# Performance work log

Measured on AMD Instinct MI355X. Metric: run time of the kernel, lower is better.

Reference implementation:

```python
import jax, jax.numpy as jnp
import numpy as np

N = 50000      # nodes
E = 600000     # edges (avg degree 12)
D = 128        # in_dim == hidden_dim
C = 47         # n_classes
L = 3          # n_layers


def setup_inputs() -> dict:
    key = jax.random.key(0)
    ks = jax.random.split(key, 8)
    s = 1.0 / np.sqrt(D)
    return {
        "features": jax.random.normal(ks[0], (N, D), jnp.float32),
        "src": jax.random.randint(ks[1], (E,), 0, N, jnp.int32),
        "dst": jax.random.randint(ks[2], (E,), 0, N, jnp.int32),
        "w_self": jax.random.normal(ks[3], (L, D, D), jnp.float32) * s,
        "w_neigh": jax.random.normal(ks[4], (L, D, D), jnp.float32) * s,
        "b": jax.random.normal(ks[5], (L, D), jnp.float32) * s,
        "wc": jax.random.normal(ks[6], (D, C), jnp.float32) * s,
        "bc": jax.random.normal(ks[7], (C,), jnp.float32) * s,
    }


def reference(features, src, dst, w_self, w_neigh, b, wc, bc):
    # in-degree for mean aggregation (clamped to avoid div-by-zero)
    deg = jax.ops.segment_sum(jnp.ones((E,), features.dtype), dst, num_segments=N)
    inv_deg = 1.0 / jnp.maximum(deg, 1.0)  # [N]
    h = features
    for l in range(L):
        # SAGEConv (mean aggregator): gather src feats, mean-reduce onto dst
        msgs = jnp.take(h, src, axis=0)                       # [E, D]
        h_neigh = jax.ops.segment_sum(msgs, dst, num_segments=N) * inv_deg[:, None]  # [N, D]
        h = jax.nn.relu(h @ w_self[l] + h_neigh @ w_neigh[l] + b[l])
    logits = h @ wc + bc                                      # [N, C]
    return jax.nn.softmax(logits, axis=-1)
```

## Files before the change

kernel.cpp:

```cpp
#include <hip/hip_runtime.h>
#include <hip/hip_bf16.h>
#include <float.h>

#define DIM  128
#define NCLS 47
#define MAXD 64

typedef __attribute__((ext_vector_type(8))) short bf16x8;
typedef __attribute__((ext_vector_type(4))) float f32x4;
typedef unsigned short u16;

__device__ inline unsigned short bf16_rne(float v) {
  unsigned u = __float_as_uint(v);
  return (unsigned short)((u + 0x7FFFu + ((u >> 16) & 1u)) >> 16);
}

__device__ inline void split_bf16(float v, unsigned short& hi, unsigned short& lo) {
  unsigned int u = __float_as_uint(v);
  unsigned int r = (u + 0x7FFFu + ((u >> 16) & 1u)) >> 16;
  hi = (unsigned short)r;
  float hf = __uint_as_float(r << 16);
  float l = v - hf;
  unsigned int ul = __float_as_uint(l);
  unsigned int rl = (ul + 0x7FFFu + ((ul >> 16) & 1u)) >> 16;
  lo = (unsigned short)rl;
}

__device__ inline uint4 pack8(const unsigned short* h) {
  uint4 u;
  u.x = (unsigned)h[0] | ((unsigned)h[1] << 16);
  u.y = (unsigned)h[2] | ((unsigned)h[3] << 16);
  u.z = (unsigned)h[4] | ((unsigned)h[5] << 16);
  u.w = (unsigned)h[6] | ((unsigned)h[7] << 16);
  return u;
}

__global__ __launch_bounds__(256) void k_init(u16* __restrict__ eidx,
                                              int* __restrict__ cnt,
                                              u16* __restrict__ P0,
                                              u16* __restrict__ P1,
                                              u16* __restrict__ P2,
                                              int n, long t8) {
  long i = (long)blockIdx.x * 256 + threadIdx.x;
  if (i < t8) {
    unsigned s2 = (unsigned)n | ((unsigned)n << 16);
    uint4 v = {s2, s2, s2, s2};
    ((uint4*)eidx)[i] = v;
  }
  if (i < n) cnt[i] = 0;
  if (i < 16) {
    uint4 z = {0u, 0u, 0u, 0u};
    ((uint4*)(P0 + (size_t)n * DIM))[i] = z;
    ((uint4*)(P1 + (size_t)n * DIM))[i] = z;
    ((uint4*)(P2 + (size_t)n * DIM))[i] = z;
  }
}

__global__ __launch_bounds__(256) void k_prep(const float* __restrict__ w_self,
                                              const float* __restrict__ w_neigh,
                                              const float* __restrict__ wc,
                                              const float* __restrict__ feat,
                                              const int* __restrict__ src,
                                              const int* __restrict__ dst,
                                              uint4* __restrict__ Bhi,
                                              uint4* __restrict__ Blo,
                                              uint4* __restrict__ Chi,
                                              uint4* __restrict__ Clo,
                                              unsigned short* __restrict__ P0,
                                              int* __restrict__ cnt,
                                              u16* __restrict__ eidx,
                                              int n, long total8, int E, int nS) {
  int bid = blockIdx.x, tid = threadIdx.x;
  if (bid < nS) {
    int t = bid * 256 + tid;
    int e0 = t * 4;
    if (e0 + 3 < E) {
      int4 d4 = *(const int4*)(dst + e0);
      int4 s4 = *(const int4*)(src + e0);
      int p0 = atomicAdd(&cnt[d4.x], 1);
      int p1 = atomicAdd(&cnt[d4.y], 1);
      int p2 = atomicAdd(&cnt[d4.z], 1);
      int p3 = atomicAdd(&cnt[d4.w], 1);
      if (p0 < MAXD) eidx[(size_t)d4.x * MAXD + p0] = (u16)s4.x;
      if (p1 < MAXD) eidx[(size_t)d4.y * MAXD + p1] = (u16)s4.y;
      if (p2 < MAXD) eidx[(size_t)d4.z * MAXD + p2] = (u16)s4.z;
      if (p3 < MAXD) eidx[(size_t)d4.w * MAXD + p3] = (u16)s4.w;
    } else {
      for (int e = e0; e < E; ++e) {
        int d = dst[e];
        int pos = atomicAdd(&cnt[d], 1);
        if (pos < MAXD) eidx[(size_t)d * MAXD + pos] = (u16)src[e];
      }
    }
    return;
  }
  bid -= nS;
  if (bid < 48) {
    int unit = bid * 4 + (tid >> 6);
    int lane = tid & 63;
    int lt = unit >> 6, rem = unit & 63, kt = rem >> 3, ct = rem & 7;
    int col = ct * 16 + (lane & 15);
    unsigned short h[8], lw[8];
#pragma unroll
    for (int j = 0; j < 8; ++j) {
      int kg = kt * 32 + (lane >> 4) * 8 + j;
      float v = (kg < 128) ? w_self[(size_t)lt * DIM * DIM + (size_t)kg * DIM + col]
                           : w_neigh[(size_t)lt * DIM * DIM + (size_t)(kg - 128) * DIM + col];
      split_bf16(v, h[j], lw[j]);
    }
    size_t idx = (((size_t)lt * 64 + kt * 8 + ct) * 64 + lane);
    Bhi[idx] = pack8(h);
    Blo[idx] = pack8(lw);
  } else if (bid < 51) {
    int unit = (bid - 48) * 4 + (tid >> 6);
    if (unit < 12) {
      int lane = tid & 63;
      int kt = unit / 3, ct = unit % 3;
      int col = ct * 16 + (lane & 15);
      unsigned short h[8], lw[8];
#pragma unroll
      for (int j = 0; j < 8; ++j) {
        int k = kt * 32 + (lane >> 4) * 8 + j;
        float v = (col < NCLS) ? wc[(size_t)k * NCLS + col] : 0.f;
        split_bf16(v, h[j], lw[j]);
      }
      size_t idx = (size_t)(kt * 3 + ct) * 64 + lane;
      Chi[idx] = pack8(h);
      Clo[idx] = pack8(lw);
    }
  } else {
    long i = (long)(bid - 51) * 256 + tid;
    if (i < total8) {
      const float* s = feat + i * 8;
      unsigned short h[8];
#pragma unroll
      for (int j = 0; j < 8; ++j) h[j] = bf16_rne(s[j]);
      *(uint4*)&P0[i * 8] = pack8(h);
    }
  }
}

__global__ __launch_bounds__(256) void k_agg9(const unsigned short* __restrict__ plane,
                                              unsigned short* __restrict__ hn,
                                              const int* __restrict__ cnt,
                                              const u16* __restrict__ eidx, int n) {
  int node = blockIdx.x * 4 + (threadIdx.x >> 6);
  if (node >= n) return;
  int lane = threadIdx.x & 63;
  int g = lane >> 4, li = lane & 15;
  int d = cnt[node];
  int dcl = d < MAXD ? d : MAXD;
  int s = node * MAXD;
  int nch = (dcl + 15) >> 4;
  float acc[8];
#pragma unroll
  for (int k = 0; k < 8; ++k) acc[k] = 0.f;

  for (int c = 0; c < nch; ++c) {
    int base = s + c * 16 + g;
    int u0 = eidx[base];
    int u1 = eidx[base + 4];
    int u2 = eidx[base + 8];
    int u3 = eidx[base + 12];
    uint4 v0 = *(const uint4*)(plane + (size_t)u0 * DIM + li * 8);
    uint4 v1 = *(const uint4*)(plane + (size_t)u1 * DIM + li * 8);
    uint4 v2 = *(const uint4*)(plane + (size_t)u2 * DIM + li * 8);
    uint4 v3 = *(const uint4*)(plane + (size_t)u3 * DIM + li * 8);
    acc[0] += __uint_as_float(v0.x << 16); acc[1] += __uint_as_float(v0.x & 0xffff0000u);
    acc[2] += __uint_as_float(v0.y << 16); acc[3] += __uint_as_float(v0.y & 0xffff0000u);
    acc[4] += __uint_as_float(v0.z << 16); acc[5] += __uint_as_float(v0.z & 0xffff0000u);
    acc[6] += __uint_as_float(v0.w << 16); acc[7] += __uint_as_float(v0.w & 0xffff0000u);
    acc[0] += __uint_as_float(v1.x << 16); acc[1] += __uint_as_float(v1.x & 0xffff0000u);
    acc[2] += __uint_as_float(v1.y << 16); acc[3] += __uint_as_float(v1.y & 0xffff0000u);
    acc[4] += __uint_as_float(v1.z << 16); acc[5] += __uint_as_float(v1.z & 0xffff0000u);
    acc[6] += __uint_as_float(v1.w << 16); acc[7] += __uint_as_float(v1.w & 0xffff0000u);
    acc[0] += __uint_as_float(v2.x << 16); acc[1] += __uint_as_float(v2.x & 0xffff0000u);
    acc[2] += __uint_as_float(v2.y << 16); acc[3] += __uint_as_float(v2.y & 0xffff0000u);
    acc[4] += __uint_as_float(v2.z << 16); acc[5] += __uint_as_float(v2.z & 0xffff0000u);
    acc[6] += __uint_as_float(v2.w << 16); acc[7] += __uint_as_float(v2.w & 0xffff0000u);
    acc[0] += __uint_as_float(v3.x << 16); acc[1] += __uint_as_float(v3.x & 0xffff0000u);
    acc[2] += __uint_as_float(v3.y << 16); acc[3] += __uint_as_float(v3.y & 0xffff0000u);
    acc[4] += __uint_as_float(v3.z << 16); acc[5] += __uint_as_float(v3.z & 0xffff0000u);
    acc[6] += __uint_as_float(v3.w << 16); acc[7] += __uint_as_float(v3.w & 0xffff0000u);
  }
#pragma unroll
  for (int k = 0; k < 8; ++k) {
    acc[k] += __shfl_xor(acc[k], 16);
    acc[k] += __shfl_xor(acc[k], 32);
  }
  if (g == 0) {
    float idg = 1.0f / (float)(d > 1 ? d : 1);
    unsigned short hb[8];
#pragma unroll
    for (int k = 0; k < 8; ++k) hb[k] = bf16_rne(acc[k] * idg);
    *(uint4*)(hn + (size_t)node * DIM + li * 8) = pack8(hb);
  }
}

template <int LAST>
__global__ __launch_bounds__(256) void k_mm2(const unsigned short* __restrict__ plane,
                                             const unsigned short* __restrict__ hn,
                                             const uint4* __restrict__ Bhi,
                                             const uint4* __restrict__ Blo,
                                             const float* __restrict__ bias,
                                             unsigned short* __restrict__ oplane,
                                             const uint4* __restrict__ Chi,
                                             const uint4* __restrict__ Clo,
                                             const float* __restrict__ bc,
                                             float* __restrict__ out,
                                             int n) {
  __shared__ char U[34816];
  uint4* Bs = (uint4*)U;
  int tid = threadIdx.x, lane = tid & 63, w = tid >> 6;
  int rb = blockIdx.x * 128 + w * 32;

  f32x4 acc[2][8];
#pragma unroll
  for (int rf = 0; rf < 2; ++rf)
#pragma unroll
    for (int ct = 0; ct < 8; ++ct) acc[rf][ct] = (f32x4){0.f, 0.f, 0.f, 0.f};

  int r0 = rb + (lane & 15);      if (r0 > n - 1) r0 = n - 1;
  int r1 = rb + 16 + (lane & 15); if (r1 > n - 1) r1 = n - 1;
  int koff = (lane >> 4) * 8;
  const unsigned short* a0s = plane + (size_t)r0 * DIM + koff;
  const unsigned short* a1s = plane + (size_t)r1 * DIM + koff;
  const unsigned short* a0n = hn + (size_t)r0 * DIM + koff;
  const unsigned short* a1n = hn + (size_t)r1 * DIM + koff;

#define STAGE_B(kt_, buf_)                                                    \
  {                                                                           \
    const uint4* hsrc = Bhi + (size_t)(kt_) * 512;                            \
    const uint4* lsrc = Blo + (size_t)(kt_) * 512;                            \
    uint4* dstb = Bs + (size_t)(buf_) * 1024;                                 \
    dstb[tid]        = hsrc[tid];                                             \
    dstb[tid + 256]  = hsrc[tid + 256];                                       \
    dstb[tid + 512]  = lsrc[tid];                                             \
    dstb[tid + 768]  = lsrc[tid + 256];                                       \
  }

  STAGE_B(0, 0);
  __syncthreads();

#pragma unroll
  for (int kt = 0; kt < 8; ++kt) {
    if (kt < 7) STAGE_B(kt + 1, (kt + 1) & 1);
    int buf = kt & 1;
    bf16x8 a0 = (kt < 4) ? *(const bf16x8*)(a0s + kt * 32)
                         : *(const bf16x8*)(a0n + (kt - 4) * 32);
    bf16x8 a1 = (kt < 4) ? *(const bf16x8*)(a1s + kt * 32)
                         : *(const bf16x8*)(a1n + (kt - 4) * 32);
    const uint4* bb = Bs + (size_t)buf * 1024;
#pragma unroll
    for (int ct = 0; ct < 8; ++ct) {
      bf16x8 bh = *(const bf16x8*)&bb[ct * 64 + lane];
      bf16x8 bl = *(const bf16x8*)&bb[512 + ct * 64 + lane];
      acc[0][ct] = __builtin_amdgcn_mfma_f32_16x16x32_bf16(a0, bh, acc[0][ct], 0, 0, 0);
      acc[0][ct] = __builtin_amdgcn_mfma_f32_16x16x32_bf16(a0, bl, acc[0][ct], 0, 0, 0);
      acc[1][ct] = __builtin_amdgcn_mfma_f32_16x16x32_bf16(a1, bh, acc[1][ct], 0, 0, 0);
      acc[1][ct] = __builtin_amdgcn_mfma_f32_16x16x32_bf16(a1, bl, acc[1][ct], 0, 0, 0);
    }
    __syncthreads();
  }
#undef STAGE_B

  char* tw = U + (size_t)w * 32 * 272;
#pragma unroll
  for (int rf = 0; rf < 2; ++rf)
#pragma unroll
    for (int ct = 0; ct < 8; ++ct) {
      float bv = bias[ct * 16 + (lane & 15)];
#pragma unroll
      for (int q = 0; q < 4; ++q) {
        float val = fmaxf(acc[rf][ct][q] + bv, 0.f);
        int row = rf * 16 + (lane >> 4) * 4 + q;
        int key = ((row >> 2) & 3) << 5;
        int cb = (ct * 32 + (lane & 15) * 2) ^ key;
        *(unsigned short*)(tw + row * 272 + cb) = bf16_rne(val);
      }
    }

  if (!LAST) {
#pragma unroll
    for (int rr = 0; rr < 2; ++rr) {
      int r = rr * 16 + (lane >> 2);
      int grow = rb + r;
      if (grow < n) {
        int key = ((r >> 2) & 3) << 5;
        int cb0 = (lane & 3) * 64;
#pragma unroll
        for (int j = 0; j < 4; ++j) {
          uint4 v = *(const uint4*)(tw + r * 272 + ((cb0 + j * 16) ^ key));
          *(uint4*)(oplane + (size_t)grow * DIM + (cb0 + j * 16) / 2) = v;
        }
      }
    }
  } else {
#pragma unroll
    for (int rf = 0; rf < 2; ++rf) {
      f32x4 cacc[3];
#pragma unroll
      for (int ct = 0; ct < 3; ++ct) cacc[ct] = (f32x4){0.f, 0.f, 0.f, 0.f};
      int row = rf * 16 + (lane & 15);
      int key = ((row >> 2) & 3) << 5;
#pragma unroll
      for (int kt = 0; kt < 4; ++kt) {
        int bo = (kt * 64 + (lane >> 4) * 16) ^ key;
        bf16x8 a = *(const bf16x8*)(tw + row * 272 + bo);
#pragma unroll
        for (int ct = 0; ct < 3; ++ct) {
          bf16x8 bh = *(const bf16x8*)&Chi[(size_t)(kt * 3 + ct) * 64 + lane];
          bf16x8 bl = *(const bf16x8*)&Clo[(size_t)(kt * 3 + ct) * 64 + lane];
          cacc[ct] = __builtin_amdgcn_mfma_f32_16x16x32_bf16(a, bh, cacc[ct], 0, 0, 0);
          cacc[ct] = __builtin_amdgcn_mfma_f32_16x16x32_bf16(a, bl, cacc[ct], 0, 0, 0);
        }
      }
      int c0 = (lane & 15);
      int c1 = 16 + (lane & 15);
      int c2 = 32 + (lane & 15);
      bool v2 = c2 < NCLS;
      float b0 = bc[c0], b1 = bc[c1], b2 = v2 ? bc[c2] : 0.f;
#pragma unroll
      for (int q = 0; q < 4; ++q) {
        int grow = rb + rf * 16 + (lane >> 4) * 4 + q;
        float l0 = cacc[0][q] + b0;
        float l1 = cacc[1][q] + b1;
        float l2 = v2 ? cacc[2][q] + b2 : -FLT_MAX;
        float m = fmaxf(l0, fmaxf(l1, l2));
#pragma unroll
        for (int off = 8; off >= 1; off >>= 1) m = fmaxf(m, __shfl_xor(m, off));
        float e0 = __expf(l0 - m);
        float e1 = __expf(l1 - m);
        float e2 = v2 ? __expf(l2 - m) : 0.f;
        float sden = e0 + e1 + e2;
#pragma unroll
        for (int off = 8; off >= 1; off >>= 1) sden += __shfl_xor(sden, off);
        float inv = 1.0f / sden;
        if (grow < n) {
          out[(size_t)grow * NCLS + c0] = e0 * inv;
          out[(size_t)grow * NCLS + c1] = e1 * inv;
          if (v2) out[(size_t)grow * NCLS + c2] = e2 * inv;
        }
      }
    }
  }
}

extern "C" void kernel_launch(void* const* d_in, const int* in_sizes, int n_in,
                              void* d_out, int out_size, void* d_ws, size_t ws_size,
                              hipStream_t stream) {
  const float* feat   = (const float*)d_in[0];
  const int*   src    = (const int*)d_in[1];
  const int*   dst    = (const int*)d_in[2];
  const float* w_self = (const float*)d_in[3];
  const float* w_neigh= (const float*)d_in[4];
  const float* b      = (const float*)d_in[5];
  const float* wc     = (const float*)d_in[6];
  const float* bc     = (const float*)d_in[7];
  float* out = (float*)d_out;

  const int N = in_sizes[0] / DIM;
  const int E = in_sizes[1];
  const size_t PS  = (size_t)N * DIM;
  const size_t PSP = (size_t)(N + 1) * DIM;

  unsigned short* P0 = (unsigned short*)d_ws;
  unsigned short* P1 = P0 + PSP;
  unsigned short* P2 = P1 + PSP;
  unsigned short* HN = P2 + PSP;
  int*   cnt  = (int*)(HN + PS);
  u16*   eidx = (u16*)(cnt + N);
  uintptr_t aln = ((uintptr_t)(eidx + (size_t)N * MAXD) + 255) & ~(uintptr_t)255;
  uint4* Bhi = (uint4*)aln;
  uint4* Blo = Bhi + 3 * 4096;
  uint4* Chi = Blo + 3 * 4096;
  uint4* Clo = Chi + 12 * 64;

  long t8 = (long)N * MAXD / 8;
  int nInit = (int)((t8 + 255) / 256);
  k_init<<<nInit, 256, 0, stream>>>(eidx, cnt, P0, P1, P2, N, t8);

  long total8 = (long)(PS / 8);
  int nCvt = (int)((total8 + 255) / 256);
  int nE4 = (E + 3) / 4;
  int nS = (nE4 + 255) / 256;
  k_prep<<<nS + 51 + nCvt, 256, 0, stream>>>(w_self, w_neigh, wc, feat, src, dst,
                                             Bhi, Blo, Chi, Clo, P0,
                                             cnt, eidx, N, total8, E, nS);

  const unsigned short* hin = P0;
  unsigned short* houts[2] = {P1, P2};
  for (int l = 0; l < 3; ++l) {
    k_agg9<<<(N + 3) / 4, 256, 0, stream>>>(hin, HN, cnt, eidx, N);
    if (l < 2) {
      k_mm2<0><<<(N + 127) / 128, 256, 0, stream>>>(hin, HN,
          Bhi + (size_t)l * 4096, Blo + (size_t)l * 4096,
          b + (size_t)l * DIM, houts[l], Chi, Clo, bc, out, N);
      hin = houts[l];
    } else {
      k_mm2<1><<<(N + 127) / 128, 256, 0, stream>>>(hin, HN,
          Bhi + (size_t)l * 4096, Blo + (size_t)l * 4096,
          b + (size_t)l * DIM, (unsigned short*)nullptr, Chi, Clo, bc, out, N);
    }
  }
}
```

Before: 177.2 us.

## Bucket neighbor lists by source-id range to improve gather locality

Each destination's neighbor list is now split into 8 buckets keyed on the high bits of the source id (16 slots each), with per-bucket atomic counters replacing the single counter. The aggregation kernel walks the buckets in order, so concurrently running wavefronts tend to gather from similar source-id ranges, which should improve L2 locality of feature reads. In exchange the index array and counters get larger, the per-node init work grows, and the inner gather loop loses its 4-way unrolled independent loads. Edges overflowing a 16-slot bucket are dropped, and nodes with more than 8 buckets' worth of ids (N beyond 65536) would overflow the layout.

```diff
diff --git a/kernel.cpp b/kernel.cpp
--- a/kernel.cpp
+++ b/kernel.cpp
@@ -2,9 +2,11 @@
 #include <hip/hip_bf16.h>
 #include <float.h>
 
-#define DIM  128
-#define NCLS 47
-#define MAXD 64
+#define DIM   128
+#define NCLS  47
+#define NBKT  8
+#define BSLOT 16
+#define SLOTS 128
 
 typedef __attribute__((ext_vector_type(8))) short bf16x8;
 typedef __attribute__((ext_vector_type(4))) float f32x4;
@@ -36,7 +38,7 @@
 }
 
 __global__ __launch_bounds__(256) void k_init(u16* __restrict__ eidx,
-                                              int* __restrict__ cnt,
+                                              int* __restrict__ cnt8,
                                               u16* __restrict__ P0,
                                               u16* __restrict__ P1,
                                               u16* __restrict__ P2,
@@ -47,7 +49,7 @@
     uint4 v = {s2, s2, s2, s2};
     ((uint4*)eidx)[i] = v;
   }
-  if (i < n) cnt[i] = 0;
+  if (i < (long)n * NBKT) cnt8[i] = 0;
   if (i < 16) {
     uint4 z = {0u, 0u, 0u, 0u};
     ((uint4*)(P0 + (size_t)n * DIM))[i] = z;
@@ -67,7 +69,7 @@
                                               uint4* __restrict__ Chi,
                                               uint4* __restrict__ Clo,
                                               unsigned short* __restrict__ P0,
-                                              int* __restrict__ cnt,
+                                              int* __restrict__ cnt8,
                                               u16* __restrict__ eidx,
                                               int n, long total8, int E, int nS) {
   int bid = blockIdx.x, tid = threadIdx.x;
@@ -77,19 +79,21 @@
     if (e0 + 3 < E) {
       int4 d4 = *(const int4*)(dst + e0);
       int4 s4 = *(const int4*)(src + e0);
-      int p0 = atomicAdd(&cnt[d4.x], 1);
-      int p1 = atomicAdd(&cnt[d4.y], 1);
-      int p2 = atomicAdd(&cnt[d4.z], 1);
-      int p3 = atomicAdd(&cnt[d4.w], 1);
-      if (p0 < MAXD) eidx[(size_t)d4.x * MAXD + p0] = (u16)s4.x;
-      if (p1 < MAXD) eidx[(size_t)d4.y * MAXD + p1] = (u16)s4.y;
-      if (p2 < MAXD) eidx[(size_t)d4.z * MAXD + p2] = (u16)s4.z;
-      if (p3 < MAXD) eidx[(size_t)d4.w * MAXD + p3] = (u16)s4.w;
+      int b0 = s4.x >> 13, b1 = s4.y >> 13, b2 = s4.z >> 13, b3 = s4.w >> 13;
+      int p0 = atomicAdd(&cnt8[(size_t)d4.x * NBKT + b0], 1);
+      int p1 = atomicAdd(&cnt8[(size_t)d4.y * NBKT + b1], 1);
+      int p2 = atomicAdd(&cnt8[(size_t)d4.z * NBKT + b2], 1);
+      int p3 = atomicAdd(&cnt8[(size_t)d4.w * NBKT + b3], 1);
+      if (p0 < BSLOT) eidx[(size_t)d4.x * SLOTS + b0 * BSLOT + p0] = (u16)s4.x;
+      if (p1 < BSLOT) eidx[(size_t)d4.y * SLOTS + b1 * BSLOT + p1] = (u16)s4.y;
+      if (p2 < BSLOT) eidx[(size_t)d4.z * SLOTS + b2 * BSLOT + p2] = (u16)s4.z;
+      if (p3 < BSLOT) eidx[(size_t)d4.w * SLOTS + b3 * BSLOT + p3] = (u16)s4.w;
     } else {
       for (int e = e0; e < E; ++e) {
-        int d = dst[e];
-        int pos = atomicAdd(&cnt[d], 1);
-        if (pos < MAXD) eidx[(size_t)d * MAXD + pos] = (u16)src[e];
+        int d = dst[e], s = src[e];
+        int b = s >> 13;
+        int pos = atomicAdd(&cnt8[(size_t)d * NBKT + b], 1);
+        if (pos < BSLOT) eidx[(size_t)d * SLOTS + b * BSLOT + pos] = (u16)s;
       }
     }
     return;
@@ -140,48 +144,39 @@
   }
 }
 
-__global__ __launch_bounds__(256) void k_agg9(const unsigned short* __restrict__ plane,
+__global__ __launch_bounds__(256) void k_aggB(const unsigned short* __restrict__ plane,
                                               unsigned short* __restrict__ hn,
-                                              const int* __restrict__ cnt,
-                                              const u16* __restrict__ eidx, int n) {
+                                              const int* __restrict__ cnt8,
+                                              const u16* __restrict__ eidx,
+                                              int n, int nb) {
   int node = blockIdx.x * 4 + (threadIdx.x >> 6);
   if (node >= n) return;
   int lane = threadIdx.x & 63;
   int g = lane >> 4, li = lane & 15;
-  int d = cnt[node];
-  int dcl = d < MAXD ? d : MAXD;
-  int s = node * MAXD;
-  int nch = (dcl + 15) >> 4;
+  const int* cb = cnt8 + (size_t)node * NBKT;
+  int c[NBKT];
+  int d = 0;
+#pragma unroll
+  for (int b = 0; b < NBKT; ++b) { c[b] = cb[b]; d += c[b]; }
+
   float acc[8];
 #pragma unroll
   for (int k = 0; k < 8; ++k) acc[k] = 0.f;
 
-  for (int c = 0; c < nch; ++c) {
-    int base = s + c * 16 + g;
-    int u0 = eidx[base];
-    int u1 = eidx[base + 4];
-    int u2 = eidx[base + 8];
-    int u3 = eidx[base + 12];
-    uint4 v0 = *(const uint4*)(plane + (size_t)u0 * DIM + li * 8);
-    uint4 v1 = *(const uint4*)(plane + (size_t)u1 * DIM + li * 8);
-    uint4 v2 = *(const uint4*)(plane + (size_t)u2 * DIM + li * 8);
-    uint4 v3 = *(const uint4*)(plane + (size_t)u3 * DIM + li * 8);
-    acc[0] += __uint_as_float(v0.x << 16); acc[1] += __uint_as_float(v0.x & 0xffff0000u);
-    acc[2] += __uint_as_float(v0.y << 16); acc[3] += __uint_as_float(v0.y & 0xffff0000u);
-    acc[4] += __uint_as_float(v0.z << 16); acc[5] += __uint_as_float(v0.z & 0xffff0000u);
-    acc[6] += __uint_as_float(v0.w << 16); acc[7] += __uint_as_float(v0.w & 0xffff0000u);
-    acc[0] += __uint_as_float(v1.x << 16); acc[1] += __uint_as_float(v1.x & 0xffff0000u);
-    acc[2] += __uint_as_float(v1.y << 16); acc[3] += __uint_as_float(v1.y & 0xffff0000u);
-    acc[4] += __uint_as_float(v1.z << 16); acc[5] += __uint_as_float(v1.z & 0xffff0000u);
-    acc[6] += __uint_as_float(v1.w << 16); acc[7] += __uint_as_float(v1.w & 0xffff0000u);
-    acc[0] += __uint_as_float(v2.x << 16); acc[1] += __uint_as_float(v2.x & 0xffff0000u);
-    acc[2] += __uint_as_float(v2.y << 16); acc[3] += __uint_as_float(v2.y & 0xffff0000u);
-    acc[4] += __uint_as_float(v2.z << 16); acc[5] += __uint_as_float(v2.z & 0xffff0000u);
-    acc[6] += __uint_as_float(v2.w << 16); acc[7] += __uint_as_float(v2.w & 0xffff0000u);
-    acc[0] += __uint_as_float(v3.x << 16); acc[1] += __uint_as_float(v3.x & 0xffff0000u);
-    acc[2] += __uint_as_float(v3.y << 16); acc[3] += __uint_as_float(v3.y & 0xffff0000u);
-    acc[4] += __uint_as_float(v3.z << 16); acc[5] += __uint_as_float(v3.z & 0xffff0000u);
-    acc[6] += __uint_as_float(v3.w << 16); acc[7] += __uint_as_float(v3.w & 0xffff0000u);
+  int base = node * SLOTS;
+  for (int b = 0; b < nb; ++b) {
+    int cbk = c[b];
+    if (cbk == 0) continue;
+    int cc = cbk < BSLOT ? cbk : BSLOT;
+    int sb = base + b * BSLOT + g;
+    for (int c0 = 0; c0 < cc; c0 += 4) {
+      int u = eidx[sb + c0];
+      uint4 v = *(const uint4*)(plane + (size_t)u * DIM + li * 8);
+      acc[0] += __uint_as_float(v.x << 16); acc[1] += __uint_as_float(v.x & 0xffff0000u);
+      acc[2] += __uint_as_float(v.y << 16); acc[3] += __uint_as_float(v.y & 0xffff0000u);
+      acc[4] += __uint_as_float(v.z << 16); acc[5] += __uint_as_float(v.z & 0xffff0000u);
+      acc[6] += __uint_as_float(v.w << 16); acc[7] += __uint_as_float(v.w & 0xffff0000u);
+    }
   }
 #pragma unroll
   for (int k = 0; k < 8; ++k) {
@@ -368,17 +363,17 @@
   unsigned short* P1 = P0 + PSP;
   unsigned short* P2 = P1 + PSP;
   unsigned short* HN = P2 + PSP;
-  int*   cnt  = (int*)(HN + PS);
-  u16*   eidx = (u16*)(cnt + N);
-  uintptr_t aln = ((uintptr_t)(eidx + (size_t)N * MAXD) + 255) & ~(uintptr_t)255;
+  int*   cnt8 = (int*)(HN + PS);
+  u16*   eidx = (u16*)(cnt8 + (size_t)N * NBKT);
+  uintptr_t aln = ((uintptr_t)(eidx + (size_t)N * SLOTS) + 255) & ~(uintptr_t)255;
   uint4* Bhi = (uint4*)aln;
   uint4* Blo = Bhi + 3 * 4096;
   uint4* Chi = Blo + 3 * 4096;
   uint4* Clo = Chi + 12 * 64;
 
-  long t8 = (long)N * MAXD / 8;
+  long t8 = (long)N * SLOTS / 8;
   int nInit = (int)((t8 + 255) / 256);
-  k_init<<<nInit, 256, 0, stream>>>(eidx, cnt, P0, P1, P2, N, t8);
+  k_init<<<nInit, 256, 0, stream>>>(eidx, cnt8, P0, P1, P2, N, t8);
 
   long total8 = (long)(PS / 8);
   int nCvt = (int)((total8 + 255) / 256);
@@ -386,12 +381,13 @@
   int nS = (nE4 + 255) / 256;
   k_prep<<<nS + 51 + nCvt, 256, 0, stream>>>(w_self, w_neigh, wc, feat, src, dst,
                                              Bhi, Blo, Chi, Clo, P0,
-                                             cnt, eidx, N, total8, E, nS);
-
+                                             cnt8, eidx, N, total8, E, nS);
+
+  int nb = (N + 8191) >> 13;
   const unsigned short* hin = P0;
   unsigned short* houts[2] = {P1, P2};
   for (int l = 0; l < 3; ++l) {
-    k_agg9<<<(N + 3) / 4, 256, 0, stream>>>(hin, HN, cnt, eidx, N);
+    k_aggB<<<(N + 3) / 4, 256, 0, stream>>>(hin, HN, cnt8, eidx, N, nb);
     if (l < 2) {
       k_mm2<0><<<(N + 127) / 128, 256, 0, stream>>>(hin, HN,
           Bhi + (size_t)l * 4096, Blo + (size_t)l * 4096,
```

Result: slower. 236.6 us (+33.6%).

## Fuse neighbor mean aggregation into the MFMA layer kernel via LDS

Applied to the files above, without the earlier changes.

Removes the separate aggregation kernel. Each 128-row matmul block now gathers and mean-reduces its own nodes' neighbor features and writes the result into a swizzled LDS tile, which then feeds the second half of the K loop. This drops the global write and read of the aggregated buffer and three kernel launches. In exchange, LDS per block grows to 64KB and the gather runs on only a few hundred blocks, with each wave handling two nodes at a time. That cuts occupancy and the parallelism available to hide gather latency.

```diff
diff --git a/kernel.cpp b/kernel.cpp
--- a/kernel.cpp
+++ b/kernel.cpp
@@ -140,93 +140,31 @@
   }
 }
 
-__global__ __launch_bounds__(256) void k_agg9(const unsigned short* __restrict__ plane,
-                                              unsigned short* __restrict__ hn,
-                                              const int* __restrict__ cnt,
-                                              const u16* __restrict__ eidx, int n) {
-  int node = blockIdx.x * 4 + (threadIdx.x >> 6);
-  if (node >= n) return;
-  int lane = threadIdx.x & 63;
-  int g = lane >> 4, li = lane & 15;
-  int d = cnt[node];
-  int dcl = d < MAXD ? d : MAXD;
-  int s = node * MAXD;
-  int nch = (dcl + 15) >> 4;
-  float acc[8];
-#pragma unroll
-  for (int k = 0; k < 8; ++k) acc[k] = 0.f;
-
-  for (int c = 0; c < nch; ++c) {
-    int base = s + c * 16 + g;
-    int u0 = eidx[base];
-    int u1 = eidx[base + 4];
-    int u2 = eidx[base + 8];
-    int u3 = eidx[base + 12];
-    uint4 v0 = *(const uint4*)(plane + (size_t)u0 * DIM + li * 8);
-    uint4 v1 = *(const uint4*)(plane + (size_t)u1 * DIM + li * 8);
-    uint4 v2 = *(const uint4*)(plane + (size_t)u2 * DIM + li * 8);
-    uint4 v3 = *(const uint4*)(plane + (size_t)u3 * DIM + li * 8);
-    acc[0] += __uint_as_float(v0.x << 16); acc[1] += __uint_as_float(v0.x & 0xffff0000u);
-    acc[2] += __uint_as_float(v0.y << 16); acc[3] += __uint_as_float(v0.y & 0xffff0000u);
-    acc[4] += __uint_as_float(v0.z << 16); acc[5] += __uint_as_float(v0.z & 0xffff0000u);
-    acc[6] += __uint_as_float(v0.w << 16); acc[7] += __uint_as_float(v0.w & 0xffff0000u);
-    acc[0] += __uint_as_float(v1.x << 16); acc[1] += __uint_as_float(v1.x & 0xffff0000u);
-    acc[2] += __uint_as_float(v1.y << 16); acc[3] += __uint_as_float(v1.y & 0xffff0000u);
-    acc[4] += __uint_as_float(v1.z << 16); acc[5] += __uint_as_float(v1.z & 0xffff0000u);
-    acc[6] += __uint_as_float(v1.w << 16); acc[7] += __uint_as_float(v1.w & 0xffff0000u);
-    acc[0] += __uint_as_float(v2.x << 16); acc[1] += __uint_as_float(v2.x & 0xffff0000u);
-    acc[2] += __uint_as_float(v2.y << 16); acc[3] += __uint_as_float(v2.y & 0xffff0000u);
-    acc[4] += __uint_as_float(v2.z << 16); acc[5] += __uint_as_float(v2.z & 0xffff0000u);
-    acc[6] += __uint_as_float(v2.w << 16); acc[7] += __uint_as_float(v2.w & 0xffff0000u);
-    acc[0] += __uint_as_float(v3.x << 16); acc[1] += __uint_as_float(v3.x & 0xffff0000u);
-    acc[2] += __uint_as_float(v3.y << 16); acc[3] += __uint_as_float(v3.y & 0xffff0000u);
-    acc[4] += __uint_as_float(v3.z << 16); acc[5] += __uint_as_float(v3.z & 0xffff0000u);
-    acc[6] += __uint_as_float(v3.w << 16); acc[7] += __uint_as_float(v3.w & 0xffff0000u);
-  }
-#pragma unroll
-  for (int k = 0; k < 8; ++k) {
-    acc[k] += __shfl_xor(acc[k], 16);
-    acc[k] += __shfl_xor(acc[k], 32);
-  }
-  if (g == 0) {
-    float idg = 1.0f / (float)(d > 1 ? d : 1);
-    unsigned short hb[8];
-#pragma unroll
-    for (int k = 0; k < 8; ++k) hb[k] = bf16_rne(acc[k] * idg);
-    *(uint4*)(hn + (size_t)node * DIM + li * 8) = pack8(hb);
-  }
-}
+#define ACC8(A, V)                                                             \
+  A[0] += __uint_as_float((V).x << 16); A[1] += __uint_as_float((V).x & 0xffff0000u); \
+  A[2] += __uint_as_float((V).y << 16); A[3] += __uint_as_float((V).y & 0xffff0000u); \
+  A[4] += __uint_as_float((V).z << 16); A[5] += __uint_as_float((V).z & 0xffff0000u); \
+  A[6] += __uint_as_float((V).w << 16); A[7] += __uint_as_float((V).w & 0xffff0000u);
 
 template <int LAST>
-__global__ __launch_bounds__(256) void k_mm2(const unsigned short* __restrict__ plane,
-                                             const unsigned short* __restrict__ hn,
-                                             const uint4* __restrict__ Bhi,
-                                             const uint4* __restrict__ Blo,
-                                             const float* __restrict__ bias,
-                                             unsigned short* __restrict__ oplane,
-                                             const uint4* __restrict__ Chi,
-                                             const uint4* __restrict__ Clo,
-                                             const float* __restrict__ bc,
-                                             float* __restrict__ out,
-                                             int n) {
-  __shared__ char U[34816];
+__global__ __launch_bounds__(256) void k_fused(const unsigned short* __restrict__ plane,
+                                               const int* __restrict__ cnt,
+                                               const u16* __restrict__ eidx,
+                                               const uint4* __restrict__ Bhi,
+                                               const uint4* __restrict__ Blo,
+                                               const float* __restrict__ bias,
+                                               unsigned short* __restrict__ oplane,
+                                               const uint4* __restrict__ Chi,
+                                               const uint4* __restrict__ Clo,
+                                               const float* __restrict__ bc,
+                                               float* __restrict__ out,
+                                               int n) {
+  __shared__ char U[65536];
   uint4* Bs = (uint4*)U;
+  char* HNl = U + 32768;
   int tid = threadIdx.x, lane = tid & 63, w = tid >> 6;
-  int rb = blockIdx.x * 128 + w * 32;
-
-  f32x4 acc[2][8];
-#pragma unroll
-  for (int rf = 0; rf < 2; ++rf)
-#pragma unroll
-    for (int ct = 0; ct < 8; ++ct) acc[rf][ct] = (f32x4){0.f, 0.f, 0.f, 0.f};
-
-  int r0 = rb + (lane & 15);      if (r0 > n - 1) r0 = n - 1;
-  int r1 = rb + 16 + (lane & 15); if (r1 > n - 1) r1 = n - 1;
-  int koff = (lane >> 4) * 8;
-  const unsigned short* a0s = plane + (size_t)r0 * DIM + koff;
-  const unsigned short* a1s = plane + (size_t)r1 * DIM + koff;
-  const unsigned short* a0n = hn + (size_t)r0 * DIM + koff;
-  const unsigned short* a1n = hn + (size_t)r1 * DIM + koff;
+  int rb = blockIdx.x * 128;
+  int wrb = rb + w * 32;
 
 #define STAGE_B(kt_, buf_)                                                    \
   {                                                                           \
@@ -240,16 +178,121 @@
   }
 
   STAGE_B(0, 0);
+
+  {
+    int g = lane >> 4, li = lane & 15;
+    for (int ii = 0; ii < 16; ++ii) {
+      int la = w * 32 + ii, lb = la + 16;
+      int na = rb + la, nb = rb + lb;
+      bool va = na < n, vb = nb < n;
+      int da = 0, db = 0;
+      uint4 av0, av1, av2, av3, bv0, bv1, bv2, bv3;
+      if (va) {
+        da = cnt[na];
+        int sa = na * MAXD + g;
+        int u0 = eidx[sa], u1 = eidx[sa + 4], u2 = eidx[sa + 8], u3 = eidx[sa + 12];
+        av0 = *(const uint4*)(plane + (size_t)u0 * DIM + li * 8);
+        av1 = *(const uint4*)(plane + (size_t)u1 * DIM + li * 8);
+        av2 = *(const uint4*)(plane + (size_t)u2 * DIM + li * 8);
+        av3 = *(const uint4*)(plane + (size_t)u3 * DIM + li * 8);
+      }
+      if (vb) {
+        db = cnt[nb];
+        int sb = nb * MAXD + g;
+        int u0 = eidx[sb], u1 = eidx[sb + 4], u2 = eidx[sb + 8], u3 = eidx[sb + 12];
+        bv0 = *(const uint4*)(plane + (size_t)u0 * DIM + li * 8);
+        bv1 = *(const uint4*)(plane + (size_t)u1 * DIM + li * 8);
+        bv2 = *(const uint4*)(plane + (size_t)u2 * DIM + li * 8);
+        bv3 = *(const uint4*)(plane + (size_t)u3 * DIM + li * 8);
+      }
+      if (va) {
+        float aa[8];
+#pragma unroll
+        for (int k = 0; k < 8; ++k) aa[k] = 0.f;
+        ACC8(aa, av0) ACC8(aa, av1) ACC8(aa, av2) ACC8(aa, av3)
+        int dcl = da < MAXD ? da : MAXD;
+        int nch = (dcl + 15) >> 4;
+        for (int c = 1; c < nch; ++c) {
+          int base = na * MAXD + c * 16 + g;
+          int u0 = eidx[base], u1 = eidx[base + 4], u2 = eidx[base + 8], u3 = eidx[base + 12];
+          uint4 v0 = *(const uint4*)(plane + (size_t)u0 * DIM + li * 8);
+          uint4 v1 = *(const uint4*)(plane + (size_t)u1 * DIM + li * 8);
+          uint4 v2 = *(const uint4*)(plane + (size_t)u2 * DIM + li * 8);
+          uint4 v3 = *(const uint4*)(plane + (size_t)u3 * DIM + li * 8);
+          ACC8(aa, v0) ACC8(aa, v1) ACC8(aa, v2) ACC8(aa, v3)
+        }
+#pragma unroll
+        for (int k = 0; k < 8; ++k) {
+          aa[k] += __shfl_xor(aa[k], 16);
+          aa[k] += __shfl_xor(aa[k], 32);
+        }
+        if (g == 0) {
+          float idg = 1.0f / (float)(da > 1 ? da : 1);
+          unsigned short hb[8];
+#pragma unroll
+          for (int k = 0; k < 8; ++k) hb[k] = bf16_rne(aa[k] * idg);
+          *(uint4*)(HNl + la * 256 + ((li * 16) ^ ((la & 7) << 4))) = pack8(hb);
+        }
+      }
+      if (vb) {
+        float ab[8];
+#pragma unroll
+        for (int k = 0; k < 8; ++k) ab[k] = 0.f;
+        ACC8(ab, bv0) ACC8(ab, bv1) ACC8(ab, bv2) ACC8(ab, bv3)
+        int dcl = db < MAXD ? db : MAXD;
+        int nch = (dcl + 15) >> 4;
+        for (int c = 1; c < nch; ++c) {
+          int base = nb * MAXD + c * 16 + g;
+          int u0 = eidx[base], u1 = eidx[base + 4], u2 = eidx[base + 8], u3 = eidx[base + 12];
+          uint4 v0 = *(const uint4*)(plane + (size_t)u0 * DIM + li * 8);
+          uint4 v1 = *(const uint4*)(plane + (size_t)u1 * DIM + li * 8);
+          uint4 v2 = *(const uint4*)(plane + (size_t)u2 * DIM + li * 8);
+          uint4 v3 = *(const uint4*)(plane + (size_t)u3 * DIM + li * 8);
+          ACC8(ab, v0) ACC8(ab, v1) ACC8(ab, v2) ACC8(ab, v3)
+        }
+#pragma unroll
+        for (int k = 0; k < 8; ++k) {
+          ab[k] += __shfl_xor(ab[k], 16);
+          ab[k] += __shfl_xor(ab[k], 32);
+        }
+        if (g == 0) {
+          float idg = 1.0f / (float)(db > 1 ? db : 1);
+          unsigned short hb[8];
+#pragma unroll
+          for (int k = 0; k < 8; ++k) hb[k] = bf16_rne(ab[k] * idg);
+          *(uint4*)(HNl + lb * 256 + ((li * 16) ^ ((lb & 7) << 4))) = pack8(hb);
+        }
+      }
+    }
+  }
   __syncthreads();
+
+  f32x4 acc[2][8];
+#pragma unroll
+  for (int rf = 0; rf < 2; ++rf)
+#pragma unroll
+    for (int ct = 0; ct < 8; ++ct) acc[rf][ct] = (f32x4){0.f, 0.f, 0.f, 0.f};
+
+  int r0 = wrb + (lane & 15);      if (r0 > n - 1) r0 = n - 1;
+  int r1 = wrb + 16 + (lane & 15); if (r1 > n - 1) r1 = n - 1;
+  int lr0 = r0 - rb, lr1 = r1 - rb;
+  int koff = (lane >> 4) * 8;
+  const unsigned short* a0s = plane + (size_t)r0 * DIM + koff;
+  const unsigned short* a1s = plane + (size_t)r1 * DIM + koff;
 
 #pragma unroll
   for (int kt = 0; kt < 8; ++kt) {
     if (kt < 7) STAGE_B(kt + 1, (kt + 1) & 1);
     int buf = kt & 1;
-    bf16x8 a0 = (kt < 4) ? *(const bf16x8*)(a0s + kt * 32)
-                         : *(const bf16x8*)(a0n + (kt - 4) * 32);
-    bf16x8 a1 = (kt < 4) ? *(const bf16x8*)(a1s + kt * 32)
-                         : *(const bf16x8*)(a1n + (kt - 4) * 32);
+    bf16x8 a0, a1;
+    if (kt < 4) {
+      a0 = *(const bf16x8*)(a0s + kt * 32);
+      a1 = *(const bf16x8*)(a1s + kt * 32);
+    } else {
+      int cb2 = koff * 2 + (kt - 4) * 64;
+      a0 = *(const bf16x8*)(HNl + lr0 * 256 + (cb2 ^ ((lr0 & 7) << 4)));
+      a1 = *(const bf16x8*)(HNl + lr1 * 256 + (cb2 ^ ((lr1 & 7) << 4)));
+    }
     const uint4* bb = Bs + (size_t)buf * 1024;
 #pragma unroll
     for (int ct = 0; ct < 8; ++ct) {
@@ -284,7 +327,7 @@
 #pragma unroll
     for (int rr = 0; rr < 2; ++rr) {
       int r = rr * 16 + (lane >> 2);
-      int grow = rb + r;
+      int grow = wrb + r;
       if (grow < n) {
         int key = ((r >> 2) & 3) << 5;
         int cb0 = (lane & 3) * 64;
@@ -322,7 +365,7 @@
       float b0 = bc[c0], b1 = bc[c1], b2 = v2 ? bc[c2] : 0.f;
 #pragma unroll
       for (int q = 0; q < 4; ++q) {
-        int grow = rb + rf * 16 + (lane >> 4) * 4 + q;
+        int grow = wrb + rf * 16 + (lane >> 4) * 4 + q;
         float l0 = cacc[0][q] + b0;
         float l1 = cacc[1][q] + b1;
         float l2 = v2 ? cacc[2][q] + b2 : -FLT_MAX;
@@ -367,8 +410,7 @@
   unsigned short* P0 = (unsigned short*)d_ws;
   unsigned short* P1 = P0 + PSP;
   unsigned short* P2 = P1 + PSP;
-  unsigned short* HN = P2 + PSP;
-  int*   cnt  = (int*)(HN + PS);
+  int*   cnt  = (int*)(P2 + PSP);
   u16*   eidx = (u16*)(cnt + N);
   uintptr_t aln = ((uintptr_t)(eidx + (size_t)N * MAXD) + 255) & ~(uintptr_t)255;
   uint4* Bhi = (uint4*)aln;
@@ -388,17 +430,17 @@
                                              Bhi, Blo, Chi, Clo, P0,
                                              cnt, eidx, N, total8, E, nS);
 
+  int nBlk = (N + 127) / 128;
   const unsigned short* hin = P0;
   unsigned short* houts[2] = {P1, P2};
   for (int l = 0; l < 3; ++l) {
-    k_agg9<<<(N + 3) / 4, 256, 0, stream>>>(hin, HN, cnt, eidx, N);
     if (l < 2) {
-      k_mm2<0><<<(N + 127) / 128, 256, 0, stream>>>(hin, HN,
+      k_fused<0><<<nBlk, 256, 0, stream>>>(hin, cnt, eidx,
           Bhi + (size_t)l * 4096, Blo + (size_t)l * 4096,
           b + (size_t)l * DIM, houts[l], Chi, Clo, bc, out, N);
       hin = houts[l];
     } else {
-      k_mm2<1><<<(N + 127) / 128, 256, 0, stream>>>(hin, HN,
+      k_fused<1><<<nBlk, 256, 0, stream>>>(hin, cnt, eidx,
           Bhi + (size_t)l * 4096, Blo + (size_t)l * 4096,
           b + (size_t)l * DIM, (unsigned short*)nullptr, Chi, Clo, bc, out, N);
     }
```

Result: slower. 220.6 us (+24.5%).

## Build neighbor lists via two-pass binned scatter with shared-memory atomics

Applied to the files above, without the earlier changes.

Replaces the direct global atomic per-edge insertion into the padded neighbor table with a two-stage binning: edges are first bucketed by dst>>8 into per-bin buffers using shared-memory histograms and one global atomic per bin per block, then a per-bin kernel assigns slots with shared atomics and writes eidx and degree counts. This aims to cut contended global atomics and scattered writes during graph preprocessing. It adds an extra kernel launch and a staging buffer with a fixed per-bin capacity that could drop edges if a bin overflows.

```diff
diff --git a/kernel.cpp b/kernel.cpp
--- a/kernel.cpp
+++ b/kernel.cpp
@@ -2,9 +2,10 @@
 #include <hip/hip_bf16.h>
 #include <float.h>
 
-#define DIM  128
-#define NCLS 47
-#define MAXD 64
+#define DIM    128
+#define NCLS   47
+#define MAXD   64
+#define BINCAP 8192
 
 typedef __attribute__((ext_vector_type(8))) short bf16x8;
 typedef __attribute__((ext_vector_type(4))) float f32x4;
@@ -36,7 +37,7 @@
 }
 
 __global__ __launch_bounds__(256) void k_init(u16* __restrict__ eidx,
-                                              int* __restrict__ cnt,
+                                              int* __restrict__ binCnt,
                                               u16* __restrict__ P0,
                                               u16* __restrict__ P1,
                                               u16* __restrict__ P2,
@@ -47,7 +48,7 @@
     uint4 v = {s2, s2, s2, s2};
     ((uint4*)eidx)[i] = v;
   }
-  if (i < n) cnt[i] = 0;
+  if (i < 4096) binCnt[i] = 0;
   if (i < 16) {
     uint4 z = {0u, 0u, 0u, 0u};
     ((uint4*)(P0 + (size_t)n * DIM))[i] = z;
@@ -56,60 +57,72 @@
   }
 }
 
-__global__ __launch_bounds__(256) void k_prep(const float* __restrict__ w_self,
-                                              const float* __restrict__ w_neigh,
-                                              const float* __restrict__ wc,
-                                              const float* __restrict__ feat,
-                                              const int* __restrict__ src,
-                                              const int* __restrict__ dst,
-                                              uint4* __restrict__ Bhi,
-                                              uint4* __restrict__ Blo,
-                                              uint4* __restrict__ Chi,
-                                              uint4* __restrict__ Clo,
-                                              unsigned short* __restrict__ P0,
-                                              int* __restrict__ cnt,
-                                              u16* __restrict__ eidx,
-                                              int n, long total8, int E, int nS) {
+__global__ __launch_bounds__(256) void k_prepS1(const float* __restrict__ w_self,
+                                                const float* __restrict__ w_neigh,
+                                                const float* __restrict__ wc,
+                                                const float* __restrict__ feat,
+                                                const int* __restrict__ src,
+                                                const int* __restrict__ dst,
+                                                uint4* __restrict__ Bhi,
+                                                uint4* __restrict__ Blo,
+                                                uint4* __restrict__ Chi,
+                                                uint4* __restrict__ Clo,
+                                                unsigned short* __restrict__ P0,
+                                                int* __restrict__ binCnt,
+                                                unsigned* __restrict__ binbuf,
+                                                int n, long total8, int E, int nS1) {
   int bid = blockIdx.x, tid = threadIdx.x;
-  if (bid < nS) {
-    int t = bid * 256 + tid;
-    int e0 = t * 4;
-    if (e0 + 3 < E) {
-      int4 d4 = *(const int4*)(dst + e0);
-      int4 s4 = *(const int4*)(src + e0);
-      int p0 = atomicAdd(&cnt[d4.x], 1);
-      int p1 = atomicAdd(&cnt[d4.y], 1);
-      int p2 = atomicAdd(&cnt[d4.z], 1);
-      int p3 = atomicAdd(&cnt[d4.w], 1);
-      if (p0 < MAXD) eidx[(size_t)d4.x * MAXD + p0] = (u16)s4.x;
-      if (p1 < MAXD) eidx[(size_t)d4.y * MAXD + p1] = (u16)s4.y;
-      if (p2 < MAXD) eidx[(size_t)d4.z * MAXD + p2] = (u16)s4.z;
-      if (p3 < MAXD) eidx[(size_t)d4.w * MAXD + p3] = (u16)s4.w;
-    } else {
-      for (int e = e0; e < E; ++e) {
-        int d = dst[e];
-        int pos = atomicAdd(&cnt[d], 1);
-        if (pos < MAXD) eidx[(size_t)d * MAXD + pos] = (u16)src[e];
+  if (bid < nS1) {
+    __shared__ int h[256], r[256], base[256];
+    h[tid] = 0; r[tid] = 0;
+    __syncthreads();
+    unsigned rec[16];
+    int e0 = bid * 4096 + tid;
+#pragma unroll
+    for (int j = 0; j < 16; ++j) {
+      int e = e0 + j * 256;
+      unsigned v = 0xFFFFFFFFu;
+      if (e < E) {
+        int d = dst[e], s = src[e];
+        v = ((unsigned)d << 16) | (unsigned)s;
+        atomicAdd(&h[d >> 8], 1);
+      }
+      rec[j] = v;
+    }
+    __syncthreads();
+    {
+      int c = h[tid];
+      base[tid] = (c > 0) ? atomicAdd(&binCnt[tid * 16], c) : 0;
+    }
+    __syncthreads();
+#pragma unroll
+    for (int j = 0; j < 16; ++j) {
+      unsigned v = rec[j];
+      if (v != 0xFFFFFFFFu) {
+        int b = v >> 24;
+        int rk = atomicAdd(&r[b], 1);
+        int pos = base[b] + rk;
+        if (pos < BINCAP) binbuf[(size_t)b * BINCAP + pos] = v;
       }
     }
     return;
   }
-  bid -= nS;
+  bid -= nS1;
   if (bid < 48) {
     int unit = bid * 4 + (tid >> 6);
     int lane = tid & 63;
     int lt = unit >> 6, rem = unit & 63, kt = rem >> 3, ct = rem & 7;
     int col = ct * 16 + (lane & 15);
-    unsigned short h[8], lw[8];
+    unsigned short h8[8], lw[8];
 #pragma unroll
     for (int j = 0; j < 8; ++j) {
       int kg = kt * 32 + (lane >> 4) * 8 + j;
       float v = (kg < 128) ? w_self[(size_t)lt * DIM * DIM + (size_t)kg * DIM + col]
                            : w_neigh[(size_t)lt * DIM * DIM + (size_t)(kg - 128) * DIM + col];
-      split_bf16(v, h[j], lw[j]);
+      split_bf16(v, h8[j], lw[j]);
     }
     size_t idx = (((size_t)lt * 64 + kt * 8 + ct) * 64 + lane);
-    Bhi[idx] = pack8(h);
+    Bhi[idx] = pack8(h8);
     Blo[idx] = pack8(lw);
   } else if (bid < 51) {
     int unit = (bid - 48) * 4 + (tid >> 6);
@@ -117,27 +130,49 @@
       int lane = tid & 63;
       int kt = unit / 3, ct = unit % 3;
       int col = ct * 16 + (lane & 15);
-      unsigned short h[8], lw[8];
+      unsigned short h8[8], lw[8];
 #pragma unroll
       for (int j = 0; j < 8; ++j) {
         int k = kt * 32 + (lane >> 4) * 8 + j;
         float v = (col < NCLS) ? wc[(size_t)k * NCLS + col] : 0.f;
-        split_bf16(v, h[j], lw[j]);
+        split_bf16(v, h8[j], lw[j]);
       }
       size_t idx = (size_t)(kt * 3 + ct) * 64 + lane;
-      Chi[idx] = pack8(h);
+      Chi[idx] = pack8(h8);
       Clo[idx] = pack8(lw);
     }
   } else {
     long i = (long)(bid - 51) * 256 + tid;
     if (i < total8) {
       const float* s = feat + i * 8;
-      unsigned short h[8];
-#pragma unroll
-      for (int j = 0; j < 8; ++j) h[j] = bf16_rne(s[j]);
-      *(uint4*)&P0[i * 8] = pack8(h);
-    }
-  }
+      unsigned short h8[8];
+#pragma unroll
+      for (int j = 0; j < 8; ++j) h8[j] = bf16_rne(s[j]);
+      *(uint4*)&P0[i * 8] = pack8(h8);
+    }
+  }
+}
+
+__global__ __launch_bounds__(256) void k_csr(const unsigned* __restrict__ binbuf,
+                                             const int* __restrict__ binCnt,
+                                             int* __restrict__ cnt,
+                                             u16* __restrict__ eidx, int n) {
+  __shared__ int c256[256];
+  int b = blockIdx.x, tid = threadIdx.x;
+  c256[tid] = 0;
+  __syncthreads();
+  int count = binCnt[b * 16];
+  if (count > BINCAP) count = BINCAP;
+  const unsigned* rec = binbuf + (size_t)b * BINCAP;
+  for (int i = tid; i < count; i += 256) {
+    unsigned v = rec[i];
+    int d = v >> 16;
+    int rk = atomicAdd(&c256[d & 255], 1);
+    if (rk < MAXD) eidx[(size_t)d * MAXD + rk] = (u16)(v & 0xFFFFu);
+  }
+  __syncthreads();
+  int node = (b << 8) | tid;
+  if (node < n) cnt[node] = c256[tid];
 }
 
 __global__ __launch_bounds__(256) void k_agg9(const unsigned short* __restrict__ plane,
@@ -375,18 +410,22 @@
   uint4* Blo = Bhi + 3 * 4096;
   uint4* Chi = Blo + 3 * 4096;
   uint4* Clo = Chi + 12 * 64;
+  int* binCnt = (int*)(Clo + 12 * 64);
+  unsigned* binbuf = (unsigned*)(binCnt + 4096);
 
   long t8 = (long)N * MAXD / 8;
   int nInit = (int)((t8 + 255) / 256);
-  k_init<<<nInit, 256, 0, stream>>>(eidx, cnt, P0, P1, P2, N, t8);
+  k_init<<<nInit, 256, 0, stream>>>(eidx, binCnt, P0, P1, P2, N, t8);
 
   long total8 = (long)(PS / 8);
   int nCvt = (int)((total8 + 255) / 256);
-  int nE4 = (E + 3) / 4;
-  int nS = (nE4 + 255) / 256;
-  k_prep<<<nS + 51 + nCvt, 256, 0, stream>>>(w_self, w_neigh, wc, feat, src, dst,
-                                             Bhi, Blo, Chi, Clo, P0,
-                                             cnt, eidx, N, total8, E, nS);
+  int nS1 = (E + 4095) / 4096;
+  k_prepS1<<<nS1 + 51 + nCvt, 256, 0, stream>>>(w_self, w_neigh, wc, feat, src, dst,
+                                                Bhi, Blo, Chi, Clo, P0,
+                                                binCnt, binbuf, N, total8, E, nS1);
+
+  int nbins = (N + 255) >> 8;
+  k_csr<<<nbins, 256, 0, stream>>>(binbuf, binCnt, cnt, eidx, N);
 
   const unsigned short* hin = P0;
   unsigned short* houts[2] = {P1, P2};
```

Measured after the change: 164.0 us. -7.4%, faster.
